# Optimization experiments

Measured on AMD Instinct MI355X. Metric: run time of the kernel, lower is better.

Reference implementation:

```python
import jax, jax.numpy as jnp
import numpy as np

MAX_BOXES = 20
IOU_THRESHOLD = 0.1
SCORE_THRESHOLD = 0.3
NUM_CLASSES = 80
N_BOXES = 10647  # YOLOv3 @416: 3*(13^2 + 26^2 + 52^2)


def setup_inputs() -> dict:
    key = jax.random.key(0)
    k1, k2, k3 = jax.random.split(key, 3)
    # boxes in [y1, x1, y2, x2] format (what tf.image.non_max_suppression expects)
    mins = jax.random.uniform(k1, (N_BOXES, 2), minval=0.0, maxval=400.0)
    sizes = jax.random.uniform(k2, (N_BOXES, 2), minval=10.0, maxval=120.0)
    boxes = jnp.concatenate([mins, mins + sizes], axis=1)  # [N,4]
    box_scores = jax.random.uniform(k3, (N_BOXES, NUM_CLASSES))  # [N,C]
    return {"boxes": boxes, "box_scores": box_scores}


def _iou_one_vs_all(box, boxes):
    # box [4], boxes [N,4], format [y1,x1,y2,x2]
    tl = jnp.maximum(box[:2], boxes[:, :2])
    br = jnp.minimum(box[2:], boxes[:, 2:])
    inter = jnp.prod(jnp.clip(br - tl, 0.0), axis=1)
    area1 = jnp.prod(box[2:] - box[:2])
    areas = jnp.prod(boxes[:, 2:] - boxes[:, :2], axis=1)
    union = area1 + areas - inter
    return jnp.where(union > 0, inter / union, 0.0)


def _nms_single_class(boxes, scores):
    """Greedy NMS for one class. Returns padded ([MAX_BOXES] int32 indices, [MAX_BOXES] bool valid).
    Matches tf.image.non_max_suppression semantics (suppress when IoU > threshold),
    applied after the score_threshold mask (invalid scores set to -inf)."""
    n = scores.shape[0]
    s0 = jnp.where(scores >= SCORE_THRESHOLD, scores, -jnp.inf)

    def body(i, state):
        s, idxs, valid = state
        j = jnp.argmax(s)
        ok = s[j] > -jnp.inf
        iou = _iou_one_vs_all(boxes[j], boxes)  # [N]
        suppress = (iou > IOU_THRESHOLD) | (jnp.arange(n) == j)
        s = jnp.where(ok & suppress, -jnp.inf, s)
        idxs = idxs.at[i].set(jnp.where(ok, j, -1).astype(jnp.int32))
        valid = valid.at[i].set(ok)
        return (s, idxs, valid)

    init = (s0, jnp.full((MAX_BOXES,), -1, jnp.int32), jnp.zeros((MAX_BOXES,), bool))
    _, idxs, valid = jax.lax.fori_loop(0, MAX_BOXES, body, init)
    return idxs, valid


def reference(boxes, box_scores):
    # Per-class greedy NMS, vectorized over classes with vmap.
    idxs, valid = jax.vmap(_nms_single_class, in_axes=(None, 1))(boxes, box_scores)  # [C,MAX_BOXES]
    c = box_scores.shape[1]
    classes = jnp.broadcast_to(jnp.arange(c, dtype=jnp.int32)[:, None], (c, MAX_BOXES))
    classes = jnp.where(valid, classes, -1)
    batch_idx = jnp.where(valid, 0, -1).astype(jnp.int32)
    # Fixed-shape (padded) analogue of the variable-length concat in the original:
    # rows are [batch_index, class, box_index]; invalid slots are -1.
    nms_final = jnp.stack([batch_idx, classes, idxs], axis=-1).reshape(1, c * MAX_BOXES, 3)
    boxes_1 = boxes[None]                 # [1,N,4]
    box_scores_t_1 = box_scores.T[None]   # [1,C,N]
    return boxes_1, box_scores_t_1, nms_final
```

## Files before the change

kernel.cpp:

```cpp
#include <hip/hip_runtime.h>
#include <math.h>

#define N_BOXES 10647
#define NUM_CLASSES 80
#define MAX_BOXES 20
#define IOU_T 0.1f
#define SCORE_T 0.3f

#define NT 1024
#define NWAVES (NT / 64)
#define KP 11
#define WCAP 128
#define TGT 96

#define TROWS 128
#define TBLOCKS 84
#define CPBLOCKS 6
#define K1_BLOCKS (TBLOCKS + CPBLOCKS)

#define OUT_OFF_SCORES (N_BOXES * 4)
#define OUT_OFF_NMS (N_BOXES * 4 + NUM_CLASSES * N_BOXES)

#define FOR_K(OP) OP(0) OP(1) OP(2) OP(3) OP(4) OP(5) OP(6) OP(7) OP(8) OP(9) OP(10)

__device__ __forceinline__ bool iou_gt(float jy1, float jx1, float jy2,
                                       float jx2, float area_j, float4 b) {
    float ty = fmaxf(jy1, b.x);
    float tx = fmaxf(jx1, b.y);
    float by = fminf(jy2, b.z);
    float bx = fminf(jx2, b.w);
    float dy = fmaxf(__fsub_rn(by, ty), 0.0f);
    float dx = fmaxf(__fsub_rn(bx, tx), 0.0f);
    float inter = __fmul_rn(dy, dx);
    if (!(inter > 0.0f)) return false;
    float area_i = __fmul_rn(__fsub_rn(b.z, b.x), __fsub_rn(b.w, b.y));
    float uni = __fsub_rn(__fadd_rn(area_j, area_i), inter);
    float iou = (uni > 0.0f) ? __fdiv_rn(inter, uni) : 0.0f;
    return iou > IOU_T;
}

__global__ __launch_bounds__(NT) void transpose_copy_kernel(
    const float* __restrict__ boxes, const float* __restrict__ scores,
    float* __restrict__ out) {
    const int tid = threadIdx.x;
    const int b = blockIdx.x;

    if (b >= TBLOCKS) {
        for (int q = (b - TBLOCKS) * NT + tid; q < N_BOXES;
             q += CPBLOCKS * NT) {
            ((float4*)out)[q] = ((const float4*)boxes)[q];
        }
        return;
    }

    __shared__ float lds[TROWS * 81];
    const int r0 = b * TROWS;
    const int nr = min(TROWS, N_BOXES - r0);

    const int nq = nr * 20;
    for (int q = tid; q < nq; q += NT) {
        const int r = q / 20;
        const int c4 = (q - r * 20) * 4;
        float4 v = *(const float4*)(scores + (r0 + r) * NUM_CLASSES + c4);
        float* dst = &lds[r * 81 + c4];
        dst[0] = v.x;
        dst[1] = v.y;
        dst[2] = v.z;
        dst[3] = v.w;
    }
    __syncthreads();

    const int r = tid & (TROWS - 1);
    const int chi = tid >> 7;
    if (r < nr) {
        #pragma unroll
        for (int p = 0; p < 10; ++p) {
            const int c = p * 8 + chi;
            out[OUT_OFF_SCORES + c * N_BOXES + r0 + r] = lds[r * 81 + c];
        }
    }
}

__global__ __launch_bounds__(NT) void nms_kernel(
    const float* __restrict__ boxes, float* __restrict__ out) {
    const int tid = threadIdx.x;
    const int c = blockIdx.x;
    const int wave = tid >> 6;
    const int lane = tid & 63;
    const float4* boxes4 = (const float4*)boxes;
    const float* col = out + OUT_OFF_SCORES + c * N_BOXES;

    __shared__ int s_hist[2048];
    __shared__ unsigned long long s_k[WCAP];
    __shared__ float4 s_b4[WCAP];
    __shared__ unsigned long long s_ks[WCAP];
    __shared__ float4 s_bs[WCAP];
    __shared__ unsigned long long s_rk[2][NWAVES];
    __shared__ int s_out[MAX_BOXES];
    __shared__ int s_bstar, s_total, s_cnt, s_nsel;

    if (tid < MAX_BOXES) s_out[tid] = -1;
    if (tid == 0) { s_cnt = 0; s_nsel = 0; }
    s_hist[tid] = 0;
    s_hist[tid + NT] = 0;
    __syncthreads();

#define DECL_K(k) unsigned long long k_##k = 0;
    FOR_K(DECL_K)
#undef DECL_K
#define BUILD_K(k)                                                     \
    {                                                                  \
        int i = tid + (k)*NT;                                          \
        if (i < N_BOXES) {                                             \
            float v = col[i];                                          \
            if (v >= SCORE_T) {                                        \
                unsigned int vb = __float_as_uint(v);                  \
                k_##k = ((unsigned long long)vb << 32) |               \
                        (0xFFFFFFFFu - (unsigned int)i);               \
                atomicAdd(&s_hist[(vb - 0x3E800000u) >> 13], 1);       \
            }                                                          \
        }                                                              \
    }
    FOR_K(BUILD_K)
#undef BUILD_K
    __syncthreads();

    if (wave == 0) {
        int lsum = 0;
        #pragma unroll
        for (int t = 0; t < 32; ++t) {
            int bb = (t + lane) & 31;
            lsum += s_hist[lane * 32 + bb];
        }
        int S = lsum;
        #pragma unroll
        for (int off = 1; off < 64; off <<= 1) {
            int up = __shfl_down(S, off);
            if (lane + off < 64) S += up;
        }
        unsigned long long mk = __ballot(S >= TGT);
        int bstar = 0;
        if (mk != 0) {
            const int L = 63 - __builtin_clzll(mk);
            const int S_L = __shfl(S, L);
            const int lsum_L = __shfl(lsum, L);
            const int S_above = S_L - lsum_L;
            int h = (lane < 32) ? s_hist[L * 32 + lane] : 0;
            int sfx = h;
            #pragma unroll
            for (int off = 1; off < 64; off <<= 1) {
                int up = __shfl_down(sfx, off);
                if (lane + off < 64) sfx += up;
            }
            unsigned long long sel = __ballot(sfx + S_above >= TGT);
            bstar = L * 32 + (63 - __builtin_clzll(sel));
        }
        if (lane == 0) {
            s_bstar = bstar;
            s_total = S;
        }
    }
    __syncthreads();

    const unsigned int tbits = 0x3E800000u + ((unsigned int)s_bstar << 13);

#define COMPACT_K(k)                                                    \
    {                                                                   \
        bool p = (k_##k != 0) &&                                        \
                 ((unsigned int)(k_##k >> 32) >= tbits);                \
        unsigned long long m = __ballot(p);                             \
        int basew = 0;                                                  \
        if (lane == 0 && m) basew = atomicAdd(&s_cnt, __popcll(m));     \
        basew = __shfl(basew, 0);                                       \
        if (p) {                                                        \
            int pos = basew + __popcll(m & ((1ull << lane) - 1ull));    \
            if (pos < WCAP) {                                           \
                s_k[pos] = k_##k;                                       \
                s_b4[pos] = boxes4[0xFFFFFFFFu - (unsigned int)k_##k];  \
            }                                                           \
        }                                                               \
    }
    FOR_K(COMPACT_K)
#undef COMPACT_K
    __syncthreads();

    const int wcnt = s_cnt;
    const bool overflow = (wcnt > WCAP);

    if (!overflow && tid < wcnt) {
        const unsigned long long mykey = s_k[tid];
        const float4 mybox = s_b4[tid];
        int rank = 0;
        for (int j = 0; j < wcnt; ++j) rank += (s_k[j] > mykey) ? 1 : 0;
        s_ks[rank] = mykey;
        s_bs[rank] = mybox;
    }
    __syncthreads();

    if (wave == 0 && !overflow && wcnt > 0) {
        int nkept = 0;
        float ky1 = 0.f, kx1 = 0.f, ky2 = 0.f, kx2 = 0.f, karea = 0.f;
        float4 bc = s_bs[0];
        unsigned long long kc = s_ks[0];
        for (int r = 0; r < wcnt; ++r) {
            const int rn = (r + 1 < wcnt) ? r + 1 : r;
            float4 bn = s_bs[rn];
            unsigned long long kn = s_ks[rn];
            bool sup = (lane < nkept) &&
                       iou_gt(ky1, kx1, ky2, kx2, karea, bc);
            if (__ballot(sup) == 0) {
                if (lane == nkept) {
                    ky1 = bc.x;
                    kx1 = bc.y;
                    ky2 = bc.z;
                    kx2 = bc.w;
                    karea = __fmul_rn(__fsub_rn(bc.z, bc.x),
                                      __fsub_rn(bc.w, bc.y));
                }
                if (lane == 0)
                    s_out[nkept] = (int)(0xFFFFFFFFu - (unsigned int)kc);
                ++nkept;
                if (nkept == MAX_BOXES) break;
            }
            bc = bn;
            kc = kn;
        }
        if (lane == 0) s_nsel = nkept;
    }
    __syncthreads();

    const int nsel0 = s_nsel;
    const bool needs_more =
        (nsel0 < MAX_BOXES) && (overflow || (wcnt < s_total));
    if (needs_more) {
#define LIVE_K(k)                                                        \
        if (k_##k != 0) {                                                \
            bool dead =                                                  \
                (!overflow &&                                            \
                 ((unsigned int)(k_##k >> 32) >= tbits));                \
            if (!dead && nsel0 > 0) {                                    \
                int i = tid + (k)*NT;                                    \
                float4 bi = boxes4[i];                                   \
                for (int j = 0; j < nsel0; ++j) {                        \
                    float4 sb = boxes4[s_out[j]];                        \
                    float aj = __fmul_rn(__fsub_rn(sb.z, sb.x),          \
                                         __fsub_rn(sb.w, sb.y));         \
                    if (iou_gt(sb.x, sb.y, sb.z, sb.w, aj, bi)) {        \
                        dead = true;                                     \
                        break;                                           \
                    }                                                    \
                }                                                        \
            }                                                            \
            if (dead) k_##k = 0;                                         \
        }
        FOR_K(LIVE_K)
#undef LIVE_K
        for (int slot = nsel0; slot < MAX_BOXES; ++slot) {
            unsigned long long bk = 0;
#define MAXK_K(k) if (k_##k > bk) bk = k_##k;
            FOR_K(MAXK_K)
#undef MAXK_K
            #pragma unroll
            for (int off = 32; off >= 1; off >>= 1) {
                unsigned long long o =
                    (unsigned long long)__shfl_xor((long long)bk, off);
                if (o > bk) bk = o;
            }
            const int par = slot & 1;
            if (lane == 0) s_rk[par][wave] = bk;
            __syncthreads();
            unsigned long long f = s_rk[par][0];
            #pragma unroll
            for (int w = 1; w < NWAVES; ++w) {
                unsigned long long o = s_rk[par][w];
                if (o > f) f = o;
            }
            if (f == 0) break;
            const int widx = (int)(0xFFFFFFFFu - (unsigned int)f);
            if (tid == 0) s_out[slot] = widx;
            float4 wb = boxes4[widx];
            const float area_j =
                __fmul_rn(__fsub_rn(wb.z, wb.x), __fsub_rn(wb.w, wb.y));
#define SCANE_K(k)                                                      \
            if (k_##k != 0) {                                           \
                int i = tid + (k)*NT;                                   \
                float4 b = boxes4[i];                                   \
                if (i == widx ||                                        \
                    iou_gt(wb.x, wb.y, wb.z, wb.w, area_j, b))          \
                    k_##k = 0;                                          \
            }
            FOR_K(SCANE_K)
#undef SCANE_K
        }
    }

    __syncthreads();
    if (tid < MAX_BOXES) {
        int bi = s_out[tid];
        int o = OUT_OFF_NMS + c * MAX_BOXES * 3 + tid * 3;
        if (bi >= 0) {
            out[o + 0] = 0.0f;
            out[o + 1] = (float)c;
            out[o + 2] = (float)bi;
        } else {
            out[o + 0] = -1.0f;
            out[o + 1] = -1.0f;
            out[o + 2] = -1.0f;
        }
    }
}

extern "C" void kernel_launch(void* const* d_in, const int* in_sizes, int n_in,
                              void* d_out, int out_size, void* d_ws,
                              size_t ws_size, hipStream_t stream) {
    const float* boxes = (const float*)d_in[0];
    const float* scores = (const float*)d_in[1];
    float* out = (float*)d_out;

    transpose_copy_kernel<<<K1_BLOCKS, NT, 0, stream>>>(boxes, scores, out);
    nms_kernel<<<NUM_CLASSES, NT, 0, stream>>>(boxes, out);
}
```

Measured before the change: 78.72 us.

## Precompute pairwise IoU suppression bitmask across all waves, then greedy select via bitmask

Replaces the serial single-wave greedy NMS over the sorted candidate window with a parallel pass where all waves compute a 128x128 IoU suppression bitmask in shared memory. Wave 0 then walks the alive bitmask with ctz and clears suppressed bits, which needs no IoU math on the serial path. The transpose kernel also halves its row tile so more blocks are launched. The cost is that every candidate pair gets an IoU computed even when only 20 are kept, plus an extra barrier.

```diff
diff --git a/kernel.cpp b/kernel.cpp
--- a/kernel.cpp
+++ b/kernel.cpp
@@ -13,8 +13,8 @@
 #define WCAP 128
 #define TGT 96
 
-#define TROWS 128
-#define TBLOCKS 84
+#define TROWS 64
+#define TBLOCKS 167
 #define CPBLOCKS 6
 #define K1_BLOCKS (TBLOCKS + CPBLOCKS)
 
@@ -71,11 +71,11 @@
     __syncthreads();
 
     const int r = tid & (TROWS - 1);
-    const int chi = tid >> 7;
+    const int chi = tid >> 6;
     if (r < nr) {
         #pragma unroll
-        for (int p = 0; p < 10; ++p) {
-            const int c = p * 8 + chi;
+        for (int p = 0; p < 5; ++p) {
+            const int c = p * 16 + chi;
             out[OUT_OFF_SCORES + c * N_BOXES + r0 + r] = lds[r * 81 + c];
         }
     }
@@ -95,6 +95,7 @@
     __shared__ float4 s_b4[WCAP];
     __shared__ unsigned long long s_ks[WCAP];
     __shared__ float4 s_bs[WCAP];
+    __shared__ __align__(16) unsigned long long s_mask[WCAP][2];
     __shared__ unsigned long long s_rk[2][NWAVES];
     __shared__ int s_out[MAX_BOXES];
     __shared__ int s_bstar, s_total, s_cnt, s_nsel;
@@ -197,33 +198,46 @@
     }
     __syncthreads();
 
-    if (wave == 0 && !overflow && wcnt > 0) {
+    if (!overflow) {
+        const int ntask = 2 * wcnt;
+        for (int t = wave; t < ntask; t += NWAVES) {
+            const int row = t >> 1, ch = t & 1;
+            float4 rb = s_bs[row];
+            float area_r =
+                __fmul_rn(__fsub_rn(rb.z, rb.x), __fsub_rn(rb.w, rb.y));
+            int colj = ch * 64 + lane;
+            bool s = (colj < wcnt) &&
+                     iou_gt(rb.x, rb.y, rb.z, rb.w, area_r, s_bs[colj]);
+            unsigned long long m = __ballot(s);
+            if (lane == 0) s_mask[row][ch] = m;
+        }
+    }
+    __syncthreads();
+
+    if (wave == 0 && !overflow) {
+        unsigned long long a0, a1;
+        if (wcnt >= 64) {
+            a0 = ~0ull;
+            a1 = (wcnt >= 128) ? ~0ull
+                               : ((wcnt > 64) ? ((1ull << (wcnt - 64)) - 1)
+                                              : 0ull);
+        } else {
+            a0 = (wcnt > 0) ? ((1ull << wcnt) - 1) : 0ull;
+            a1 = 0ull;
+        }
         int nkept = 0;
-        float ky1 = 0.f, kx1 = 0.f, ky2 = 0.f, kx2 = 0.f, karea = 0.f;
-        float4 bc = s_bs[0];
-        unsigned long long kc = s_ks[0];
-        for (int r = 0; r < wcnt; ++r) {
-            const int rn = (r + 1 < wcnt) ? r + 1 : r;
-            float4 bn = s_bs[rn];
-            unsigned long long kn = s_ks[rn];
-            bool sup = (lane < nkept) &&
-                       iou_gt(ky1, kx1, ky2, kx2, karea, bc);
-            if (__ballot(sup) == 0) {
-                if (lane == nkept) {
-                    ky1 = bc.x;
-                    kx1 = bc.y;
-                    ky2 = bc.z;
-                    kx2 = bc.w;
-                    karea = __fmul_rn(__fsub_rn(bc.z, bc.x),
-                                      __fsub_rn(bc.w, bc.y));
-                }
-                if (lane == 0)
-                    s_out[nkept] = (int)(0xFFFFFFFFu - (unsigned int)kc);
-                ++nkept;
-                if (nkept == MAX_BOXES) break;
-            }
-            bc = bn;
-            kc = kn;
+        while ((a0 | a1) != 0 && nkept < MAX_BOXES) {
+            int pos = a0 ? __builtin_ctzll(a0)
+                         : 64 + __builtin_ctzll(a1);
+            if (lane == 0)
+                s_out[nkept] =
+                    (int)(0xFFFFFFFFu - (unsigned int)s_ks[pos]);
+            ++nkept;
+            ulonglong2 m = *(const ulonglong2*)&s_mask[pos][0];
+            a0 &= ~m.x;
+            a1 &= ~m.y;
+            if (pos < 64) a0 &= ~(1ull << pos);
+            else a1 &= ~(1ull << (pos - 64));
         }
         if (lane == 0) s_nsel = nkept;
     }
```

Result: no change. 77.61 us (-1.4%).
